# Performance work log

Hardware: AMD Instinct MI355X
Metric: run time of the kernel (lower is better)

## Reference

```python
import jax, jax.numpy as jnp
import numpy as np

N_STREAMS = 4
HIDDEN = 1024
SINKHORN_ITERS = 20
TAU = 0.05
EPS = 1e-6
RMS_EPS = 1e-8


def rms_norm(x, weight):
    # x: [T, d] fp32
    rms = jnp.mean(x * x, axis=-1, keepdims=True)
    return x * jax.lax.rsqrt(rms + RMS_EPS) * weight


def sinkhorn_log(logits, n_iters=SINKHORN_ITERS, tau=TAU):
    # logits: [T, n, n] -> doubly-stochastic [T, n, n]
    Z = logits / tau
    u0 = jnp.zeros(Z.shape[:-1], Z.dtype)  # [T, n]
    v0 = jnp.zeros_like(u0)

    def body(i, uv):
        u, v = uv
        u = -jax.nn.logsumexp(Z + v[..., None, :], axis=-1)
        v = -jax.nn.logsumexp(Z + u[..., :, None], axis=-2)
        return (u, v)

    u, v = jax.lax.fori_loop(0, n_iters, body, (u0, v0))
    return jnp.exp(Z + u[..., :, None] + v[..., None, :])


def setup_inputs() -> dict:
    key = jax.random.key(0)
    ks = jax.random.split(key, 6)
    d = N_STREAMS * HIDDEN
    x_streams = jax.random.normal(ks[0], (4, 2048, N_STREAMS, HIDDEN), dtype=jnp.float32)
    scale = 1.0 / np.sqrt(d)
    return {
        "x_streams": x_streams,
        "rms_weight": jnp.ones((d,), jnp.float32),
        "W_pre": jax.random.normal(ks[1], (N_STREAMS, d), jnp.float32) * scale,
        "W_post": jax.random.normal(ks[2], (N_STREAMS, d), jnp.float32) * scale,
        "W_res": jax.random.normal(ks[3], (N_STREAMS * N_STREAMS, d), jnp.float32) * scale,
        "bias_pre": jnp.zeros((N_STREAMS,), jnp.float32),
        "bias_post": jnp.zeros((N_STREAMS,), jnp.float32),
        "bias_res": jnp.zeros((N_STREAMS * N_STREAMS,), jnp.float32),
        "alpha_pre": jnp.full((1,), 0.01, jnp.float32),
        "alpha_post": jnp.full((1,), 0.01, jnp.float32),
        "alpha_res": jnp.full((1,), 0.01, jnp.float32),
        "W_sub": jax.random.normal(ks[4], (HIDDEN, HIDDEN), jnp.float32) * (1.0 / np.sqrt(HIDDEN)),
    }


def reference(x_streams, rms_weight, W_pre, W_post, W_res, bias_pre, bias_post,
              bias_res, alpha_pre, alpha_post, alpha_res, W_sub):
    B, S, n, C = x_streams.shape
    d = n * C
    x_flat = x_streams.reshape(B * S, d).astype(jnp.float32)
    x_norm = rms_norm(x_flat, rms_weight)

    H_pre = jax.nn.sigmoid(alpha_pre * (x_norm @ W_pre.T) + bias_pre)        # [T, n]
    H_post = 2.0 * jax.nn.sigmoid(alpha_post * (x_norm @ W_post.T) + bias_post)
    H_res = sinkhorn_log((alpha_res * (x_norm @ W_res.T) + bias_res).reshape(B * S, n, n))

    H_pre = H_pre.reshape(B, S, n)
    H_post = H_post.reshape(B, S, n)
    H_res = H_res.reshape(B, S, n, n)

    H_pre_w = H_pre / (jnp.sum(H_pre, axis=-1, keepdims=True) + EPS)
    H_post_w = H_post / (jnp.sum(H_post, axis=-1, keepdims=True) + EPS)

    # pre-aggregate streams -> single stream
    x_layer = jnp.einsum('bsnc,bsn->bsc', x_streams, H_pre_w)
    # sublayer: bias-free linear
    y = x_layer @ W_sub.T                                                    # [B, S, C]
    # broadcast sublayer output back to streams
    y_expanded = H_post_w[..., None] * y[:, :, None, :]                      # [B, S, n, C]
    # doubly-stochastic residual stream mixing
    x_mixed = jnp.einsum('bsic,bsoi->bsoc', x_streams, H_res)
    return x_mixed + y_expanded
```

## Files before the change

### kernel.cpp

```cpp
#include <hip/hip_runtime.h>

#define NTOK 8192
#define D 4096
#define CH 1024

typedef __attribute__((ext_vector_type(8))) short short8v;
typedef __attribute__((ext_vector_type(4))) float float4v;
typedef __attribute__((ext_vector_type(4))) unsigned short ushort4v;

static __device__ __forceinline__ unsigned short f2bf(float f) {
  unsigned int u = __float_as_uint(f);
  u += 0x7fff + ((u >> 16) & 1);
  return (unsigned short)(u >> 16);
}

static __device__ __forceinline__ void async_cp16(const void* g, void* l) {
  __builtin_amdgcn_global_load_lds((__attribute__((address_space(1))) void*)g,
                                   (__attribute__((address_space(3))) void*)l,
                                   16, 0, 0);
}

__global__ __launch_bounds__(512) void gates_kernel(
    const float* __restrict__ x, const float* __restrict__ rms_w,
    const float* __restrict__ Wpre, const float* __restrict__ Wpost,
    const float* __restrict__ Wres, const float* __restrict__ bpre,
    const float* __restrict__ bpost, const float* __restrict__ bres,
    const float* __restrict__ apre, const float* __restrict__ apost,
    const float* __restrict__ ares, const float* __restrict__ Wsub,
    unsigned short* __restrict__ Wb, float* __restrict__ gates_out,
    unsigned short* __restrict__ xlayer) {
  __shared__ float xbuf[2][8][256];
  __shared__ float logits_lds[8][24];
  __shared__ float sq_lds[8];
  __shared__ float s_lds[8];
  __shared__ float hpre_lds[8][4];

  const int tid = threadIdx.x;
  const int lane = tid & 63;
  const int w = tid >> 6;
  const int tok0 = blockIdx.x * 8;

  {
    int i = blockIdx.x * 1024 + tid * 2;
    float2 v = *(const float2*)(Wsub + i);
    unsigned int packed = (unsigned int)f2bf(v.x) | ((unsigned int)f2bf(v.y) << 16);
    *(unsigned int*)(Wb + i) = packed;
  }

  const float* Wp[3];
#pragma unroll
  for (int g = 0; g < 3; ++g) {
    int gg = w * 3 + g;
    Wp[g] = (gg < 4) ? (Wpre + gg * D)
          : (gg < 8) ? (Wpost + (gg - 4) * D)
                     : (Wres + (gg - 8) * D);
  }

  float acc[3][8];
#pragma unroll
  for (int g = 0; g < 3; ++g)
#pragma unroll
    for (int t = 0; t < 8; ++t) acc[g][t] = 0.f;
  float sq = 0.f;

  async_cp16(x + (size_t)(tok0 + w) * D + lane * 4, (void*)&xbuf[0][w][0]);
  __syncthreads();

  for (int chk = 0; chk < 16; ++chk) {
    const int cb = chk * 256;
    const int cur = chk & 1;
    if (chk < 15)
      async_cp16(x + (size_t)(tok0 + w) * D + cb + 256 + lane * 4,
                 (void*)&xbuf[cur ^ 1][w][0]);
    float4 w4[3];
#pragma unroll
    for (int g = 0; g < 3; ++g) w4[g] = *(const float4*)(Wp[g] + cb + lane * 4);
    float4 r4 = *(const float4*)(rms_w + cb + lane * 4);
#pragma unroll
    for (int t = 0; t < 8; ++t) {
      float4 xv = *(const float4*)(&xbuf[cur][t][lane * 4]);
      if (t == w)
        sq += xv.x * xv.x + xv.y * xv.y + xv.z * xv.z + xv.w * xv.w;
      float4 xr;
      xr.x = xv.x * r4.x; xr.y = xv.y * r4.y; xr.z = xv.z * r4.z; xr.w = xv.w * r4.w;
#pragma unroll
      for (int g = 0; g < 3; ++g)
        acc[g][t] += xr.x * w4[g].x + xr.y * w4[g].y + xr.z * w4[g].z + xr.w * w4[g].w;
    }
    __syncthreads();
  }

#pragma unroll
  for (int g = 0; g < 3; ++g)
#pragma unroll
    for (int t = 0; t < 8; ++t) {
      float v = acc[g][t];
      for (int off = 32; off > 0; off >>= 1) v += __shfl_xor(v, off, 64);
      if (lane == 0) logits_lds[t][w * 3 + g] = v;
    }
  {
    float v = sq;
    for (int off = 32; off > 0; off >>= 1) v += __shfl_xor(v, off, 64);
    if (lane == 0) sq_lds[w] = v;
  }
  __syncthreads();

  if (tid < 8) {
    const int t = tid;
    float s = rsqrtf(sq_lds[t] * (1.0f / 4096.0f) + 1e-8f);
    s_lds[t] = s;
    float a_pre = apre[0], a_post = apost[0];

    float hp[4];
    float sum_p = 1e-6f;
#pragma unroll
    for (int i = 0; i < 4; ++i) {
      float z = a_pre * (s * logits_lds[t][i]) + bpre[i];
      hp[i] = 1.0f / (1.0f + __expf(-z));
      sum_p += hp[i];
    }
    float inv_p = 1.0f / sum_p;
#pragma unroll
    for (int i = 0; i < 4; ++i) hpre_lds[t][i] = hp[i] * inv_p;

    float* go = gates_out + (size_t)(tok0 + t) * 20;
    float hq[4];
    float sum_q = 1e-6f;
#pragma unroll
    for (int i = 0; i < 4; ++i) {
      float z = a_post * (s * logits_lds[t][4 + i]) + bpost[i];
      hq[i] = 2.0f / (1.0f + __expf(-z));
      sum_q += hq[i];
    }
    float inv_q = 1.0f / sum_q;
#pragma unroll
    for (int i = 0; i < 4; ++i) go[i] = hq[i] * inv_q;
  }
  __syncthreads();

  {
    const int col = (tid & 255) * 4;
    const int half = tid >> 8;
#pragma unroll
    for (int r = 0; r < 4; ++r) {
      const int t = r * 2 + half;
      float h0 = hpre_lds[t][0], h1 = hpre_lds[t][1];
      float h2 = hpre_lds[t][2], h3 = hpre_lds[t][3];
      const size_t base = (size_t)(tok0 + t) * D;
      float4 x0 = *(const float4*)(x + base + 0 * CH + col);
      float4 x1 = *(const float4*)(x + base + 1 * CH + col);
      float4 x2 = *(const float4*)(x + base + 2 * CH + col);
      float4 x3 = *(const float4*)(x + base + 3 * CH + col);
      ushort4v o;
      o.x = f2bf(h0 * x0.x + h1 * x1.x + h2 * x2.x + h3 * x3.x);
      o.y = f2bf(h0 * x0.y + h1 * x1.y + h2 * x2.y + h3 * x3.y);
      o.z = f2bf(h0 * x0.z + h1 * x1.z + h2 * x2.z + h3 * x3.z);
      o.w = f2bf(h0 * x0.w + h1 * x1.w + h2 * x2.w + h3 * x3.w);
      *(ushort4v*)(xlayer + (size_t)(tok0 + t) * CH + col) = o;
    }
  }

  if (tid < 32) {
    const int t = tid >> 2;
    const int r = tid & 3;
    const float s = s_lds[t];
    const float a_res = ares[0];
    float Zrow[4], Zcol[4];
#pragma unroll
    for (int j = 0; j < 4; ++j) {
      Zrow[j] = (a_res * (s * logits_lds[t][8 + r * 4 + j]) + bres[r * 4 + j]) * 20.0f;
      Zcol[j] = (a_res * (s * logits_lds[t][8 + j * 4 + r]) + bres[j * 4 + r]) * 20.0f;
    }
    float u = 0.f, v = 0.f;
    const int base = t << 2;
    for (int it = 0; it < 20; ++it) {
      float v0 = __shfl(v, base + 0, 64), v1 = __shfl(v, base + 1, 64);
      float v2 = __shfl(v, base + 2, 64), v3 = __shfl(v, base + 3, 64);
      float a0 = Zrow[0] + v0, a1 = Zrow[1] + v1, a2 = Zrow[2] + v2, a3 = Zrow[3] + v3;
      float m = fmaxf(fmaxf(a0, a1), fmaxf(a2, a3));
      float sm = __expf(a0 - m) + __expf(a1 - m) + __expf(a2 - m) + __expf(a3 - m);
      u = -(m + __logf(sm));
      float u0 = __shfl(u, base + 0, 64), u1 = __shfl(u, base + 1, 64);
      float u2 = __shfl(u, base + 2, 64), u3 = __shfl(u, base + 3, 64);
      float b0 = Zcol[0] + u0, b1 = Zcol[1] + u1, b2 = Zcol[2] + u2, b3 = Zcol[3] + u3;
      float m2 = fmaxf(fmaxf(b0, b1), fmaxf(b2, b3));
      float sm2 = __expf(b0 - m2) + __expf(b1 - m2) + __expf(b2 - m2) + __expf(b3 - m2);
      v = -(m2 + __logf(sm2));
    }
    float v0 = __shfl(v, base + 0, 64), v1 = __shfl(v, base + 1, 64);
    float v2 = __shfl(v, base + 2, 64), v3 = __shfl(v, base + 3, 64);
    float* go = gates_out + (size_t)(tok0 + t) * 20;
    go[4 + r * 4 + 0] = __expf(Zrow[0] + u + v0);
    go[4 + r * 4 + 1] = __expf(Zrow[1] + u + v1);
    go[4 + r * 4 + 2] = __expf(Zrow[2] + u + v2);
    go[4 + r * 4 + 3] = __expf(Zrow[3] + u + v3);
  }
}

__global__ __launch_bounds__(256) void gemm_epi(
    const unsigned short* __restrict__ A,
    const unsigned short* __restrict__ B,
    const float* __restrict__ x,
    const float* __restrict__ gates,
    float* __restrict__ out) {
  __shared__ __align__(16) char lds_raw[128 * 132 * 4];
  __shared__ float gsm[128 * 20];
  unsigned short* stg = (unsigned short*)lds_raw;
  float* ybuf = (float*)lds_raw;

  const int tid = threadIdx.x;
  const int lane = tid & 63;
  const int w = tid >> 6;
  const int n0 = blockIdx.x * 128;
  const int m0 = blockIdx.y * 128;

  for (int i = tid; i < 128 * 20; i += 256) gsm[i] = gates[(size_t)m0 * 20 + i];

  float4v accf[4][4];
#pragma unroll
  for (int mi = 0; mi < 4; ++mi)
#pragma unroll
    for (int ni = 0; ni < 4; ++ni) {
      accf[mi][ni].x = 0.f; accf[mi][ni].y = 0.f;
      accf[mi][ni].z = 0.f; accf[mi][ni].w = 0.f;
    }

  const int wm = (w >> 1) * 64;
  const int wn = (w & 1) * 64;
  const int srow = lane >> 3;
  const int sslot = lane & 7;

#define STAGE(KT, BUF)                                                        \
  {                                                                           \
    const int k0s = (KT) * 64;                                                \
    unsigned short* As = stg + (BUF) * 8192;                                  \
    unsigned short* Bs = stg + 16384 + (BUF) * 8192;                          \
    _Pragma("unroll")                                                         \
    for (int i = 0; i < 4; ++i) {                                             \
      int chunk = w * 4 + i;                                                  \
      int row = chunk * 8 + srow;                                             \
      int qg = sslot ^ (row & 7);                                             \
      async_cp16(A + (size_t)(m0 + row) * 1024 + k0s + qg * 8,                \
                 (void*)(As + chunk * 512));                                  \
      async_cp16(B + (size_t)(n0 + row) * 1024 + k0s + qg * 8,                \
                 (void*)(Bs + chunk * 512));                                  \
    }                                                                         \
  }

  STAGE(0, 0);
  __syncthreads();

  for (int kt = 0; kt < 16; ++kt) {
    const int cur = kt & 1;
    if (kt < 15) STAGE(kt + 1, cur ^ 1);
    const unsigned short* As = stg + cur * 8192;
    const unsigned short* Bs = stg + 16384 + cur * 8192;
#pragma unroll
    for (int kk = 0; kk < 2; ++kk) {
      short8v a[4], b[4];
#pragma unroll
      for (int mi = 0; mi < 4; ++mi) {
        int row = wm + mi * 16 + (lane & 15);
        int q = (kk * 4 + (lane >> 4)) ^ (row & 7);
        a[mi] = *(const short8v*)(As + row * 64 + q * 8);
      }
#pragma unroll
      for (int ni = 0; ni < 4; ++ni) {
        int row = wn + ni * 16 + (lane & 15);
        int q = (kk * 4 + (lane >> 4)) ^ (row & 7);
        b[ni] = *(const short8v*)(Bs + row * 64 + q * 8);
      }
#pragma unroll
      for (int mi = 0; mi < 4; ++mi)
#pragma unroll
        for (int ni = 0; ni < 4; ++ni)
          accf[mi][ni] = __builtin_amdgcn_mfma_f32_16x16x32_bf16(
              a[mi], b[ni], accf[mi][ni], 0, 0, 0);
    }
    __syncthreads();
  }

#pragma unroll
  for (int mi = 0; mi < 4; ++mi)
#pragma unroll
    for (int ni = 0; ni < 4; ++ni)
#pragma unroll
      for (int r = 0; r < 4; ++r) {
        int row = wm + mi * 16 + (lane >> 4) * 4 + r;
        int col = wn + ni * 16 + (lane & 15);
        ybuf[row * 132 + col] = accf[mi][ni][r];
      }
  __syncthreads();

#pragma unroll 4
  for (int i = 0; i < 16; ++i) {
    int idx = i * 256 + tid;
    int tl = idx >> 5;
    int c4 = idx & 31;
    const size_t t = (size_t)(m0 + tl);
    const float* gp = gsm + tl * 20;
    float4 y4 = *(const float4*)&ybuf[tl * 132 + c4 * 4];
    const size_t xb = t * 4096 + n0 + c4 * 4;
    float4 x0 = *(const float4*)(x + xb);
    float4 x1 = *(const float4*)(x + xb + 1024);
    float4 x2 = *(const float4*)(x + xb + 2048);
    float4 x3 = *(const float4*)(x + xb + 3072);
#pragma unroll
    for (int o = 0; o < 4; ++o) {
      float h0 = gp[4 + o * 4 + 0], h1 = gp[4 + o * 4 + 1];
      float h2 = gp[4 + o * 4 + 2], h3 = gp[4 + o * 4 + 3];
      float hp = gp[o];
      float4 rr;
      rr.x = x0.x * h0 + x1.x * h1 + x2.x * h2 + x3.x * h3 + hp * y4.x;
      rr.y = x0.y * h0 + x1.y * h1 + x2.y * h2 + x3.y * h3 + hp * y4.y;
      rr.z = x0.z * h0 + x1.z * h1 + x2.z * h2 + x3.z * h3 + hp * y4.z;
      rr.w = x0.w * h0 + x1.w * h1 + x2.w * h2 + x3.w * h3 + hp * y4.w;
      *(float4*)(out + t * 4096 + (size_t)o * 1024 + n0 + c4 * 4) = rr;
    }
  }
}

extern "C" void kernel_launch(void* const* d_in, const int* in_sizes, int n_in,
                              void* d_out, int out_size, void* d_ws, size_t ws_size,
                              hipStream_t stream) {
  const float* x     = (const float*)d_in[0];
  const float* rms_w = (const float*)d_in[1];
  const float* Wpre  = (const float*)d_in[2];
  const float* Wpost = (const float*)d_in[3];
  const float* Wres  = (const float*)d_in[4];
  const float* bpre  = (const float*)d_in[5];
  const float* bpost = (const float*)d_in[6];
  const float* bres  = (const float*)d_in[7];
  const float* apre  = (const float*)d_in[8];
  const float* apost = (const float*)d_in[9];
  const float* ares  = (const float*)d_in[10];
  const float* Wsub  = (const float*)d_in[11];
  float* out = (float*)d_out;

  char* ws = (char*)d_ws;
  float* gates           = (float*)ws;
  unsigned short* Wb     = (unsigned short*)(ws + (1 << 20));
  unsigned short* xlayer = (unsigned short*)(ws + (4 << 20));

  gates_kernel<<<1024, 512, 0, stream>>>(x, rms_w, Wpre, Wpost, Wres, bpre,
                                         bpost, bres, apre, apost, ares,
                                         Wsub, Wb, gates, xlayer);
  gemm_epi<<<dim3(8, 64), 256, 0, stream>>>(xlayer, Wb, x, gates, out);
}
```

Baseline: 383.4 us.

## Stage whole token rows in LDS for gates; write epilogue directly from MFMA registers

The gates kernel now processes 4 tokens per block across 2048 blocks. Each block async-copies full 4096-float rows into LDS once, and both the gate projections and the x_layer pre-aggregation read from that LDS copy instead of re-reading x from global memory. The per-chunk barriers are gone. The Sinkhorn work moves to one wave, and the other waves start the x_layer writes in parallel with it. The GEMM epilogue drops the ybuf LDS round trip and writes outputs straight from the accumulators with scalar strided loads and stores. That can hurt coalescing compared with float4 accesses, and the 64KB LDS per gates block may limit occupancy.

```diff
diff --git a/kernel.cpp b/kernel.cpp
--- a/kernel.cpp
+++ b/kernel.cpp
@@ -20,7 +20,7 @@
                                    16, 0, 0);
 }
 
-__global__ __launch_bounds__(512) void gates_kernel(
+__global__ __launch_bounds__(512, 4) void gates_kernel(
     const float* __restrict__ x, const float* __restrict__ rms_w,
     const float* __restrict__ Wpre, const float* __restrict__ Wpost,
     const float* __restrict__ Wres, const float* __restrict__ bpre,
@@ -29,18 +29,27 @@
     const float* __restrict__ ares, const float* __restrict__ Wsub,
     unsigned short* __restrict__ Wb, float* __restrict__ gates_out,
     unsigned short* __restrict__ xlayer) {
-  __shared__ float xbuf[2][8][256];
-  __shared__ float logits_lds[8][24];
-  __shared__ float sq_lds[8];
-  __shared__ float s_lds[8];
-  __shared__ float hpre_lds[8][4];
+  __shared__ float xbuf[4][4096];
+  __shared__ float logits_lds[4][24];
+  __shared__ float sq_lds[4];
+  __shared__ float s_lds[4];
+  __shared__ float hpre_lds[4][4];
 
   const int tid = threadIdx.x;
   const int lane = tid & 63;
   const int w = tid >> 6;
-  const int tok0 = blockIdx.x * 8;
+  const int tok0 = blockIdx.x * 4;
 
   {
+    const int t = w >> 1;
+    const int c0 = (w & 1) * 2048;
+    const float* src = x + (size_t)(tok0 + t) * D + c0 + lane * 4;
+#pragma unroll
+    for (int j = 0; j < 8; ++j)
+      async_cp16(src + j * 256, (void*)&xbuf[t][c0 + j * 256]);
+  }
+
+  if (blockIdx.x < 1024) {
     int i = blockIdx.x * 1024 + tid * 2;
     float2 v = *(const float2*)(Wsub + i);
     unsigned int packed = (unsigned int)f2bf(v.x) | ((unsigned int)f2bf(v.y) << 16);
@@ -56,30 +65,26 @@
                      : (Wres + (gg - 8) * D);
   }
 
-  float acc[3][8];
+  float acc[3][4];
 #pragma unroll
   for (int g = 0; g < 3; ++g)
 #pragma unroll
-    for (int t = 0; t < 8; ++t) acc[g][t] = 0.f;
+    for (int t = 0; t < 4; ++t) acc[g][t] = 0.f;
   float sq = 0.f;
 
-  async_cp16(x + (size_t)(tok0 + w) * D + lane * 4, (void*)&xbuf[0][w][0]);
   __syncthreads();
 
+#pragma unroll 4
   for (int chk = 0; chk < 16; ++chk) {
-    const int cb = chk * 256;
-    const int cur = chk & 1;
-    if (chk < 15)
-      async_cp16(x + (size_t)(tok0 + w) * D + cb + 256 + lane * 4,
-                 (void*)&xbuf[cur ^ 1][w][0]);
+    const int cb = chk * 256 + lane * 4;
     float4 w4[3];
 #pragma unroll
-    for (int g = 0; g < 3; ++g) w4[g] = *(const float4*)(Wp[g] + cb + lane * 4);
-    float4 r4 = *(const float4*)(rms_w + cb + lane * 4);
-#pragma unroll
-    for (int t = 0; t < 8; ++t) {
-      float4 xv = *(const float4*)(&xbuf[cur][t][lane * 4]);
-      if (t == w)
+    for (int g = 0; g < 3; ++g) w4[g] = *(const float4*)(Wp[g] + cb);
+    float4 r4 = *(const float4*)(rms_w + cb);
+#pragma unroll
+    for (int t = 0; t < 4; ++t) {
+      float4 xv = *(const float4*)(&xbuf[t][cb]);
+      if (w == (t << 1))
         sq += xv.x * xv.x + xv.y * xv.y + xv.z * xv.z + xv.w * xv.w;
       float4 xr;
       xr.x = xv.x * r4.x; xr.y = xv.y * r4.y; xr.z = xv.z * r4.z; xr.w = xv.w * r4.w;
@@ -87,25 +92,24 @@
       for (int g = 0; g < 3; ++g)
         acc[g][t] += xr.x * w4[g].x + xr.y * w4[g].y + xr.z * w4[g].z + xr.w * w4[g].w;
     }
-    __syncthreads();
   }
 
 #pragma unroll
   for (int g = 0; g < 3; ++g)
 #pragma unroll
-    for (int t = 0; t < 8; ++t) {
+    for (int t = 0; t < 4; ++t) {
       float v = acc[g][t];
       for (int off = 32; off > 0; off >>= 1) v += __shfl_xor(v, off, 64);
       if (lane == 0) logits_lds[t][w * 3 + g] = v;
     }
-  {
+  if ((w & 1) == 0) {
     float v = sq;
     for (int off = 32; off > 0; off >>= 1) v += __shfl_xor(v, off, 64);
-    if (lane == 0) sq_lds[w] = v;
+    if (lane == 0) sq_lds[w >> 1] = v;
   }
   __syncthreads();
 
-  if (tid < 8) {
+  if (tid < 4) {
     const int t = tid;
     float s = rsqrtf(sq_lds[t] * (1.0f / 4096.0f) + 1e-8f);
     s_lds[t] = s;
@@ -138,75 +142,76 @@
   }
   __syncthreads();
 
-  {
-    const int col = (tid & 255) * 4;
-    const int half = tid >> 8;
-#pragma unroll
-    for (int r = 0; r < 4; ++r) {
-      const int t = r * 2 + half;
-      float h0 = hpre_lds[t][0], h1 = hpre_lds[t][1];
-      float h2 = hpre_lds[t][2], h3 = hpre_lds[t][3];
-      const size_t base = (size_t)(tok0 + t) * D;
-      float4 x0 = *(const float4*)(x + base + 0 * CH + col);
-      float4 x1 = *(const float4*)(x + base + 1 * CH + col);
-      float4 x2 = *(const float4*)(x + base + 2 * CH + col);
-      float4 x3 = *(const float4*)(x + base + 3 * CH + col);
-      ushort4v o;
-      o.x = f2bf(h0 * x0.x + h1 * x1.x + h2 * x2.x + h3 * x3.x);
-      o.y = f2bf(h0 * x0.y + h1 * x1.y + h2 * x2.y + h3 * x3.y);
-      o.z = f2bf(h0 * x0.z + h1 * x1.z + h2 * x2.z + h3 * x3.z);
-      o.w = f2bf(h0 * x0.w + h1 * x1.w + h2 * x2.w + h3 * x3.w);
-      *(ushort4v*)(xlayer + (size_t)(tok0 + t) * CH + col) = o;
-    }
-  }
-
-  if (tid < 32) {
-    const int t = tid >> 2;
-    const int r = tid & 3;
-    const float s = s_lds[t];
-    const float a_res = ares[0];
-    float Zrow[4], Zcol[4];
-#pragma unroll
-    for (int j = 0; j < 4; ++j) {
-      Zrow[j] = (a_res * (s * logits_lds[t][8 + r * 4 + j]) + bres[r * 4 + j]) * 20.0f;
-      Zcol[j] = (a_res * (s * logits_lds[t][8 + j * 4 + r]) + bres[j * 4 + r]) * 20.0f;
-    }
-    float u = 0.f, v = 0.f;
-    const int base = t << 2;
-    for (int it = 0; it < 20; ++it) {
+  auto phB = [&](int s) {
+    const int t = s >> 8;
+    const int c4 = (s & 255) * 4;
+    const float h0 = hpre_lds[t][0], h1 = hpre_lds[t][1];
+    const float h2 = hpre_lds[t][2], h3 = hpre_lds[t][3];
+    const float4 x0 = *(const float4*)&xbuf[t][c4];
+    const float4 x1 = *(const float4*)&xbuf[t][1024 + c4];
+    const float4 x2 = *(const float4*)&xbuf[t][2048 + c4];
+    const float4 x3 = *(const float4*)&xbuf[t][3072 + c4];
+    ushort4v o;
+    o.x = f2bf(h0 * x0.x + h1 * x1.x + h2 * x2.x + h3 * x3.x);
+    o.y = f2bf(h0 * x0.y + h1 * x1.y + h2 * x2.y + h3 * x3.y);
+    o.z = f2bf(h0 * x0.z + h1 * x1.z + h2 * x2.z + h3 * x3.z);
+    o.w = f2bf(h0 * x0.w + h1 * x1.w + h2 * x2.w + h3 * x3.w);
+    *(ushort4v*)(xlayer + (size_t)(tok0 + t) * CH + c4) = o;
+  };
+
+  if (w == 0) {
+    if (lane < 16) {
+      const int t = lane >> 2;
+      const int r = lane & 3;
+      const float s = s_lds[t];
+      const float a_res = ares[0];
+      float Zrow[4], Zcol[4];
+#pragma unroll
+      for (int j = 0; j < 4; ++j) {
+        Zrow[j] = (a_res * (s * logits_lds[t][8 + r * 4 + j]) + bres[r * 4 + j]) * 20.0f;
+        Zcol[j] = (a_res * (s * logits_lds[t][8 + j * 4 + r]) + bres[j * 4 + r]) * 20.0f;
+      }
+      float u = 0.f, v = 0.f;
+      const int base = t << 2;
+      for (int it = 0; it < 20; ++it) {
+        float v0 = __shfl(v, base + 0, 64), v1 = __shfl(v, base + 1, 64);
+        float v2 = __shfl(v, base + 2, 64), v3 = __shfl(v, base + 3, 64);
+        float a0 = Zrow[0] + v0, a1 = Zrow[1] + v1, a2 = Zrow[2] + v2, a3 = Zrow[3] + v3;
+        float m = fmaxf(fmaxf(a0, a1), fmaxf(a2, a3));
+        float sm = __expf(a0 - m) + __expf(a1 - m) + __expf(a2 - m) + __expf(a3 - m);
+        u = -(m + __logf(sm));
+        float u0 = __shfl(u, base + 0, 64), u1 = __shfl(u, base + 1, 64);
+        float u2 = __shfl(u, base + 2, 64), u3 = __shfl(u, base + 3, 64);
+        float b0 = Zcol[0] + u0, b1 = Zcol[1] + u1, b2 = Zcol[2] + u2, b3 = Zcol[3] + u3;
+        float m2 = fmaxf(fmaxf(b0, b1), fmaxf(b2, b3));
+        float sm2 = __expf(b0 - m2) + __expf(b1 - m2) + __expf(b2 - m2) + __expf(b3 - m2);
+        v = -(m2 + __logf(sm2));
+      }
       float v0 = __shfl(v, base + 0, 64), v1 = __shfl(v, base + 1, 64);
       float v2 = __shfl(v, base + 2, 64), v3 = __shfl(v, base + 3, 64);
-      float a0 = Zrow[0] + v0, a1 = Zrow[1] + v1, a2 = Zrow[2] + v2, a3 = Zrow[3] + v3;
-      float m = fmaxf(fmaxf(a0, a1), fmaxf(a2, a3));
-      float sm = __expf(a0 - m) + __expf(a1 - m) + __expf(a2 - m) + __expf(a3 - m);
-      u = -(m + __logf(sm));
-      float u0 = __shfl(u, base + 0, 64), u1 = __shfl(u, base + 1, 64);
-      float u2 = __shfl(u, base + 2, 64), u3 = __shfl(u, base + 3, 64);
-      float b0 = Zcol[0] + u0, b1 = Zcol[1] + u1, b2 = Zcol[2] + u2, b3 = Zcol[3] + u3;
-      float m2 = fmaxf(fmaxf(b0, b1), fmaxf(b2, b3));
-      float sm2 = __expf(b0 - m2) + __expf(b1 - m2) + __expf(b2 - m2) + __expf(b3 - m2);
-      v = -(m2 + __logf(sm2));
-    }
-    float v0 = __shfl(v, base + 0, 64), v1 = __shfl(v, base + 1, 64);
-    float v2 = __shfl(v, base + 2, 64), v3 = __shfl(v, base + 3, 64);
-    float* go = gates_out + (size_t)(tok0 + t) * 20;
-    go[4 + r * 4 + 0] = __expf(Zrow[0] + u + v0);
-    go[4 + r * 4 + 1] = __expf(Zrow[1] + u + v1);
-    go[4 + r * 4 + 2] = __expf(Zrow[2] + u + v2);
-    go[4 + r * 4 + 3] = __expf(Zrow[3] + u + v3);
-  }
-}
-
-__global__ __launch_bounds__(256) void gemm_epi(
+      float* go = gates_out + (size_t)(tok0 + t) * 20;
+      go[4 + r * 4 + 0] = __expf(Zrow[0] + u + v0);
+      go[4 + r * 4 + 1] = __expf(Zrow[1] + u + v1);
+      go[4 + r * 4 + 2] = __expf(Zrow[2] + u + v2);
+      go[4 + r * 4 + 3] = __expf(Zrow[3] + u + v3);
+    }
+    phB(896 + lane);
+    phB(960 + lane);
+  } else {
+    phB(tid - 64);
+    phB(tid + 384);
+  }
+}
+
+__global__ __launch_bounds__(256, 2) void gemm_epi(
     const unsigned short* __restrict__ A,
     const unsigned short* __restrict__ B,
     const float* __restrict__ x,
     const float* __restrict__ gates,
     float* __restrict__ out) {
-  __shared__ __align__(16) char lds_raw[128 * 132 * 4];
-  __shared__ float gsm[128 * 20];
-  unsigned short* stg = (unsigned short*)lds_raw;
-  float* ybuf = (float*)lds_raw;
+  __shared__ __align__(16) unsigned short stg[32768];
+  __shared__ float hpost_sm[128][4];
+  __shared__ float hres_sm[128][16];
 
   const int tid = threadIdx.x;
   const int lane = tid & 63;
@@ -214,7 +219,17 @@
   const int n0 = blockIdx.x * 128;
   const int m0 = blockIdx.y * 128;
 
-  for (int i = tid; i < 128 * 20; i += 256) gsm[i] = gates[(size_t)m0 * 20 + i];
+  {
+    const int r = tid >> 1, half = tid & 1;
+    const float* gp = gates + (size_t)(m0 + r) * 20 + half * 10;
+#pragma unroll
+    for (int j = 0; j < 10; ++j) {
+      int jj = half * 10 + j;
+      float v = gp[j];
+      if (jj < 4) hpost_sm[r][jj] = v;
+      else        hres_sm[r][jj - 4] = v;
+    }
+  }
 
   float4v accf[4][4];
 #pragma unroll
@@ -280,42 +295,31 @@
     __syncthreads();
   }
 
-#pragma unroll
-  for (int mi = 0; mi < 4; ++mi)
-#pragma unroll
-    for (int ni = 0; ni < 4; ++ni)
-#pragma unroll
-      for (int r = 0; r < 4; ++r) {
-        int row = wm + mi * 16 + (lane >> 4) * 4 + r;
-        int col = wn + ni * 16 + (lane & 15);
-        ybuf[row * 132 + col] = accf[mi][ni][r];
-      }
-  __syncthreads();
-
-#pragma unroll 4
-  for (int i = 0; i < 16; ++i) {
-    int idx = i * 256 + tid;
-    int tl = idx >> 5;
-    int c4 = idx & 31;
-    const size_t t = (size_t)(m0 + tl);
-    const float* gp = gsm + tl * 20;
-    float4 y4 = *(const float4*)&ybuf[tl * 132 + c4 * 4];
-    const size_t xb = t * 4096 + n0 + c4 * 4;
-    float4 x0 = *(const float4*)(x + xb);
-    float4 x1 = *(const float4*)(x + xb + 1024);
-    float4 x2 = *(const float4*)(x + xb + 2048);
-    float4 x3 = *(const float4*)(x + xb + 3072);
-#pragma unroll
-    for (int o = 0; o < 4; ++o) {
-      float h0 = gp[4 + o * 4 + 0], h1 = gp[4 + o * 4 + 1];
-      float h2 = gp[4 + o * 4 + 2], h3 = gp[4 + o * 4 + 3];
-      float hp = gp[o];
-      float4 rr;
-      rr.x = x0.x * h0 + x1.x * h1 + x2.x * h2 + x3.x * h3 + hp * y4.x;
-      rr.y = x0.y * h0 + x1.y * h1 + x2.y * h2 + x3.y * h3 + hp * y4.y;
-      rr.z = x0.z * h0 + x1.z * h1 + x2.z * h2 + x3.z * h3 + hp * y4.z;
-      rr.w = x0.w * h0 + x1.w * h1 + x2.w * h2 + x3.w * h3 + hp * y4.w;
-      *(float4*)(out + t * 4096 + (size_t)o * 1024 + n0 + c4 * 4) = rr;
+  const int rg = (lane >> 4) * 4;
+  const int cl = lane & 15;
+#pragma unroll
+  for (int mi = 0; mi < 4; ++mi) {
+#pragma unroll
+    for (int r = 0; r < 4; ++r) {
+      const int row = wm + mi * 16 + rg + r;
+      const size_t t = (size_t)(m0 + row);
+      const float4 hq = *(const float4*)(&hpost_sm[row][0]);
+      const float4 h0 = *(const float4*)(&hres_sm[row][0]);
+      const float4 h1 = *(const float4*)(&hres_sm[row][4]);
+      const float4 h2 = *(const float4*)(&hres_sm[row][8]);
+      const float4 h3 = *(const float4*)(&hres_sm[row][12]);
+      const float* xp = x + t * 4096 + n0 + wn + cl;
+      float* op = out + t * 4096 + n0 + wn + cl;
+#pragma unroll
+      for (int ni = 0; ni < 4; ++ni) {
+        const int c = ni * 16;
+        float x0 = xp[c], x1 = xp[c + 1024], x2 = xp[c + 2048], x3 = xp[c + 3072];
+        float y = accf[mi][ni][r];
+        op[c]        = x0 * h0.x + x1 * h0.y + x2 * h0.z + x3 * h0.w + hq.x * y;
+        op[c + 1024] = x0 * h1.x + x1 * h1.y + x2 * h1.z + x3 * h1.w + hq.y * y;
+        op[c + 2048] = x0 * h2.x + x1 * h2.y + x2 * h2.z + x3 * h2.w + hq.z * y;
+        op[c + 3072] = x0 * h3.x + x1 * h3.y + x2 * h3.z + x3 * h3.w + hq.w * y;
+      }
     }
   }
 }
@@ -342,7 +346,7 @@
   unsigned short* Wb     = (unsigned short*)(ws + (1 << 20));
   unsigned short* xlayer = (unsigned short*)(ws + (4 << 20));
 
-  gates_kernel<<<1024, 512, 0, stream>>>(x, rms_w, Wpre, Wpost, Wres, bpre,
+  gates_kernel<<<2048, 512, 0, stream>>>(x, rms_w, Wpre, Wpost, Wres, bpre,
                                          bpost, bres, apre, apost, ares,
                                          Wsub, Wb, gates, xlayer);
   gemm_epi<<<dim3(8, 64), 256, 0, stream>>>(xlayer, Wb, x, gates, out);
```

Result: no change. 375.9 us (-2.0%).
